# Performance work log

Measured on AMD Instinct MI355X. Metric: run time of the kernel, lower is better.

## Reference

```python
import jax, jax.numpy as jnp
import numpy as np

N_GRAPHS = 64

def setup_inputs() -> dict:
    key = jax.random.key(0)
    ks = jax.random.split(key, 8)
    N, E, H = 50000, 600000, 128
    x = jax.random.normal(ks[0], (N, 2), dtype=jnp.float32)
    edge_index = jax.random.randint(ks[1], (2, E), 0, N, dtype=jnp.int64)
    batch = jnp.sort(jax.random.randint(ks[2], (N,), 0, N_GRAPHS, dtype=jnp.int64))
    s = 0.1  # keep tanh out of saturation
    return {
        'x': x,
        'edge_index': edge_index,
        'batch': batch,
        'W1': jax.random.normal(ks[3], (2, H), dtype=jnp.float32) * s,
        'b1': jnp.zeros((H,), jnp.float32),
        'W2': jax.random.normal(ks[4], (H, H), dtype=jnp.float32) * s,
        'b2': jnp.zeros((H,), jnp.float32),
        'W3': jax.random.normal(ks[5], (H, H), dtype=jnp.float32) * s,
        'b3': jnp.zeros((H,), jnp.float32),
        'Wo': jax.random.normal(ks[6], (2 * H, 41), dtype=jnp.float32) * s,
        'bo': jnp.zeros((41,), jnp.float32),
    }

def reference(x, edge_index, batch, W1, b1, W2, b2, W3, b3, Wo, bo):
    N = x.shape[0]
    src, dst = edge_index[0], edge_index[1]
    # GCN symmetric normalization with self loops: deg = in-degree + 1
    ones_e = jnp.ones(src.shape[0], dtype=x.dtype)
    deg = jax.ops.segment_sum(ones_e, dst, num_segments=N) + 1.0
    dinv = jax.lax.rsqrt(deg)                       # [N]
    edge_norm = (dinv[src] * dinv[dst])[:, None]    # [E,1]
    self_norm = (dinv * dinv)[:, None]              # [N,1]

    def gcn(h, W, b):
        h = h @ W                                   # [N,H] transform first
        agg = jax.ops.segment_sum(h[src] * edge_norm, dst, num_segments=N)
        return agg + h * self_norm + b

    h = jnp.tanh(gcn(x, W1, b1))
    h = jnp.tanh(gcn(h, W2, b2))
    h = jnp.tanh(gcn(h, W3, b3))

    # global max pool + global mean pool over graphs
    cnt = jax.ops.segment_sum(jnp.ones(N, dtype=h.dtype), batch, num_segments=N_GRAPHS)
    mx = jax.ops.segment_max(h, batch, num_segments=N_GRAPHS)
    mx = jnp.where(cnt[:, None] > 0, mx, 0.0)
    mean = jax.ops.segment_sum(h, batch, num_segments=N_GRAPHS) / jnp.maximum(cnt, 1.0)[:, None]
    pooled = jnp.concatenate([mx, mean], axis=1)    # [G, 2H]
    return jnp.tanh(pooled @ Wo + bo)               # [G, 41]
```

## Files before the change

### kernel.cpp

```cpp
#include <hip/hip_runtime.h>
#include <math.h>

#define NGRAPH 64
#define SCAN_BLK 1024
#define COLCAP 6144
#define AXCAP 2560

typedef short short8 __attribute__((ext_vector_type(8)));
typedef float floatx4 __attribute__((ext_vector_type(4)));

__device__ inline unsigned pack_bf16x2(float a, float b) {
    unsigned ua = __float_as_uint(a);
    unsigned ub = __float_as_uint(b);
    ua = (ua + 0x7fffu + ((ua >> 16) & 1u)) >> 16;
    ub = (ub + 0x7fffu + ((ub >> 16) & 1u)) >> 16;
    return ua | (ub << 16);
}
__device__ inline unsigned short bf16_1(float a) {
    unsigned ua = __float_as_uint(a);
    return (unsigned short)((ua + 0x7fffu + ((ua >> 16) & 1u)) >> 16);
}
__device__ inline float bf16lo(unsigned u) { return __uint_as_float(u << 16); }
__device__ inline float bf16hi(unsigned u) { return __uint_as_float(u & 0xffff0000u); }

__device__ inline unsigned fkey(float v) {
    unsigned u = __float_as_uint(v);
    return (v >= 0.f) ? (u | 0x80000000u) : ~u;
}


#define TIDX(u) ((size_t)((qb + (unsigned)(u)) * 4u + (unsigned)q))
#define ACC4() do {                                                       \
    uint4 v0 = t4[TIDX(u0)]; uint4 v1 = t4[TIDX(u1)];                     \
    uint4 v2 = t4[TIDX(u2)]; uint4 v3 = t4[TIDX(u3)];                     \
    a[0] += bf16lo(v0.x); a[1] += bf16hi(v0.x);                           \
    a[2] += bf16lo(v0.y); a[3] += bf16hi(v0.y);                           \
    a[4] += bf16lo(v0.z); a[5] += bf16hi(v0.z);                           \
    a[6] += bf16lo(v0.w); a[7] += bf16hi(v0.w);                           \
    a[0] += bf16lo(v1.x); a[1] += bf16hi(v1.x);                           \
    a[2] += bf16lo(v1.y); a[3] += bf16hi(v1.y);                           \
    a[4] += bf16lo(v1.z); a[5] += bf16hi(v1.z);                           \
    a[6] += bf16lo(v1.w); a[7] += bf16hi(v1.w);                           \
    a[0] += bf16lo(v2.x); a[1] += bf16hi(v2.x);                           \
    a[2] += bf16lo(v2.y); a[3] += bf16hi(v2.y);                           \
    a[4] += bf16lo(v2.z); a[5] += bf16hi(v2.z);                           \
    a[6] += bf16lo(v2.w); a[7] += bf16hi(v2.w);                           \
    a[0] += bf16lo(v3.x); a[1] += bf16hi(v3.x);                           \
    a[2] += bf16lo(v3.y); a[3] += bf16hi(v3.y);                           \
    a[4] += bf16lo(v3.z); a[5] += bf16hi(v3.z);                           \
    a[6] += bf16lo(v3.w); a[7] += bf16hi(v3.w);                           \
} while (0)
#define ACC4M() do {                                                      \
    uint4 v0 = t4[TIDX(u0)]; uint4 v1 = t4[TIDX(u1)];                     \
    uint4 v2 = t4[TIDX(u2)]; uint4 v3 = t4[TIDX(u3)];                     \
    a[0] += bf16lo(v0.x); a[1] += bf16hi(v0.x);                           \
    a[2] += bf16lo(v0.y); a[3] += bf16hi(v0.y);                           \
    a[4] += bf16lo(v0.z); a[5] += bf16hi(v0.z);                           \
    a[6] += bf16lo(v0.w); a[7] += bf16hi(v0.w);                           \
    a[0] = fmaf(m1, bf16lo(v1.x), a[0]); a[1] = fmaf(m1, bf16hi(v1.x), a[1]); \
    a[2] = fmaf(m1, bf16lo(v1.y), a[2]); a[3] = fmaf(m1, bf16hi(v1.y), a[3]); \
    a[4] = fmaf(m1, bf16lo(v1.z), a[4]); a[5] = fmaf(m1, bf16hi(v1.z), a[5]); \
    a[6] = fmaf(m1, bf16lo(v1.w), a[6]); a[7] = fmaf(m1, bf16hi(v1.w), a[7]); \
    a[0] = fmaf(m2, bf16lo(v2.x), a[0]); a[1] = fmaf(m2, bf16hi(v2.x), a[1]); \
    a[2] = fmaf(m2, bf16lo(v2.y), a[2]); a[3] = fmaf(m2, bf16hi(v2.y), a[3]); \
    a[4] = fmaf(m2, bf16lo(v2.z), a[4]); a[5] = fmaf(m2, bf16hi(v2.z), a[5]); \
    a[6] = fmaf(m2, bf16lo(v2.w), a[6]); a[7] = fmaf(m2, bf16hi(v2.w), a[7]); \
    a[0] = fmaf(m3, bf16lo(v3.x), a[0]); a[1] = fmaf(m3, bf16hi(v3.x), a[1]); \
    a[2] = fmaf(m3, bf16lo(v3.y), a[2]); a[3] = fmaf(m3, bf16hi(v3.y), a[3]); \
    a[4] = fmaf(m3, bf16lo(v3.z), a[4]); a[5] = fmaf(m3, bf16hi(v3.z), a[5]); \
    a[6] = fmaf(m3, bf16lo(v3.w), a[6]); a[7] = fmaf(m3, bf16hi(v3.w), a[7]); \
} while (0)


__global__ void pack_count(const int* __restrict__ dst, int E, int* __restrict__ cnt,
                           int* __restrict__ rank,
                           const float* __restrict__ W2, const float* __restrict__ W3,
                           unsigned* __restrict__ Wt2, unsigned* __restrict__ Wt3) {
    if (blockIdx.x < 32) {
        int b = blockIdx.x;
        const float* W = (b < 16) ? W2 : W3;
        unsigned* Wt = (b < 16) ? Wt2 : Wt3;
        b &= 15;
        int bk = b & 3, bn = b >> 2;
        __shared__ float s[32][33];
        int tx = threadIdx.x & 31, ty = threadIdx.x >> 5;
#pragma unroll
        for (int r = 0; r < 4; ++r)
            s[r * 8 + ty][tx] = W[(bk * 32 + r * 8 + ty) * 128 + bn * 32 + tx];
        __syncthreads();
        int t16 = threadIdx.x & 15, tn = threadIdx.x >> 4;
#pragma unroll
        for (int pass = 0; pass < 2; ++pass) {
            int nl = pass * 16 + tn;
            unsigned pk = pack_bf16x2(s[2 * t16][nl], s[2 * t16 + 1][nl]);
            Wt[(bn * 32 + nl) * 64 + bk * 16 + t16] = pk;
        }
    } else {
        int e = (blockIdx.x - 32) * blockDim.x + threadIdx.x;
        if (e < E) rank[e] = atomicAdd(&cnt[dst[e]], 1);
    }
}


__global__ __launch_bounds__(SCAN_BLK) void scanA(const int* __restrict__ cnt,
                                                  const float* __restrict__ x,
                                                  int* __restrict__ row_ptr,
                                                  int* __restrict__ bsum,
                                                  float* __restrict__ dinv,
                                                  float2* __restrict__ y,
                                                  const int* __restrict__ batch,
                                                  int* __restrict__ ticket,
                                                  int* __restrict__ goff, int N) {
    __shared__ int sm[SCAN_BLK];
    __shared__ int amLast;
    int i = blockIdx.x * SCAN_BLK + threadIdx.x;
    int v = (i < N) ? cnt[i] : 0;
    if (i < N) {
        float dv = rsqrtf((float)v + 1.0f);
        dinv[i] = dv;
        float2 xv = ((const float2*)x)[i];
        y[i] = make_float2(xv.x * dv, xv.y * dv);
    }
    sm[threadIdx.x] = v;
    __syncthreads();
    for (int off = 1; off < SCAN_BLK; off <<= 1) {
        int t = (threadIdx.x >= (unsigned)off) ? sm[threadIdx.x - off] : 0;
        __syncthreads();
        sm[threadIdx.x] += t;
        __syncthreads();
    }
    if (i < N) row_ptr[i] = sm[threadIdx.x] - v;
    if (threadIdx.x == SCAN_BLK - 1) bsum[blockIdx.x] = sm[SCAN_BLK - 1];
    __syncthreads();
    if (threadIdx.x == 0) {
        __threadfence();
        amLast = (atomicAdd(ticket, 1) == (int)gridDim.x - 1);
    }
    __syncthreads();
    if (!amLast) return;
    int nb = (int)gridDim.x;
    int v2 = (threadIdx.x < (unsigned)nb) ? atomicAdd(&bsum[threadIdx.x], 0) : 0;
    sm[threadIdx.x] = v2;
    __syncthreads();
    for (int off = 1; off < SCAN_BLK; off <<= 1) {
        int t = (threadIdx.x >= (unsigned)off) ? sm[threadIdx.x - off] : 0;
        __syncthreads();
        sm[threadIdx.x] += t;
        __syncthreads();
    }
    if (threadIdx.x < (unsigned)nb) bsum[threadIdx.x] = sm[threadIdx.x] - v2;
    if (threadIdx.x <= NGRAPH) {
        int g = threadIdx.x;
        int lo = 0, hi = N;
        while (lo < hi) {
            int mid = (lo + hi) >> 1;
            if (batch[mid] < g) lo = mid + 1; else hi = mid;
        }
        goff[g] = lo;
    }
}

__global__ void fill_kernel(const int* __restrict__ src, const int* __restrict__ dst, int E,
                            const int* __restrict__ row_ptr, const int* __restrict__ bsum,
                            const int* __restrict__ rank, int* __restrict__ col) {
    int e = blockIdx.x * blockDim.x + threadIdx.x;
    if (e < E) {
        int d = dst[e];
        int p = row_ptr[d] + bsum[d >> 10] + rank[e];
        col[p] = src[e];
    }
}


__global__ __launch_bounds__(256) void agg_x_t1(const float2* __restrict__ y,
                                                const int* __restrict__ row_ptr,
                                                const int* __restrict__ bsum,
                                                const int* __restrict__ col,
                                                const float* __restrict__ dinv,
                                                const float* __restrict__ W1,
                                                const float* __restrict__ b1,
                                                unsigned short* __restrict__ h, int N, int E) {
    __shared__ float4 sW[64];
    __shared__ float4 sb[32];
    __shared__ float2 zs[64];
    __shared__ int scol[AXCAP];
    if (threadIdx.x < 64) sW[threadIdx.x] = ((const float4*)W1)[threadIdx.x];
    if (threadIdx.x >= 64 && threadIdx.x < 96) sb[threadIdx.x - 64] = ((const float4*)b1)[threadIdx.x - 64];

    int firstNode = blockIdx.x * 64;
    int lastNode = min(firstNode + 64, N);
    int sBase = row_ptr[firstNode] + bsum[firstNode >> 10];
    int eEnd = (lastNode < N) ? row_ptr[lastNode] + bsum[lastNode >> 10] : E;
    int range = eEnd - sBase;
    bool inLds = (range <= AXCAP);
    if (inLds) {
        for (int i = threadIdx.x; i < range; i += 256) scol[i] = col[sBase + i];
    }
    __syncthreads();

    int grp = threadIdx.x >> 2;
    int l4 = threadIdx.x & 3;
    int node = firstNode + grp;
    float ax = 0.f, ay = 0.f;
    if (node < N) {
        int s = row_ptr[node] + bsum[node >> 10];
        int e = (node + 1 < N) ? row_ptr[node + 1] + bsum[(node + 1) >> 10] : E;
        int deg = e - s;
        if (inLds) {
            int sl = s - sBase;
            int j = l4;
            for (; j + 4 < deg; j += 8) {
                float2 v0 = y[scol[sl + j]];
                float2 v1 = y[scol[sl + j + 4]];
                ax += v0.x; ay += v0.y;
                ax += v1.x; ay += v1.y;
            }
            if (j < deg) { float2 v = y[scol[sl + j]]; ax += v.x; ay += v.y; }
        } else {
            int j = l4;
            for (; j + 4 < deg; j += 8) {
                float2 v0 = y[col[s + j]];
                float2 v1 = y[col[s + j + 4]];
                ax += v0.x; ay += v0.y;
                ax += v1.x; ay += v1.y;
            }
            if (j < deg) { float2 v = y[col[s + j]]; ax += v.x; ay += v.y; }
        }
    }
    ax += __shfl_xor(ax, 1, 64); ay += __shfl_xor(ay, 1, 64);
    ax += __shfl_xor(ax, 2, 64); ay += __shfl_xor(ay, 2, 64);
    if (l4 == 0 && node < N) {
        float2 self = y[node];
        float dv = dinv[node];
        zs[grp] = make_float2(dv * (ax + self.x), dv * (ay + self.y));
    }
    __syncthreads();

    int q = threadIdx.x & 31;
    int rsub = threadIdx.x >> 5;
    float4 w0 = sW[q];
    float4 w1 = sW[32 + q];
    float4 b = sb[q];
    size_t qoff = (size_t)(q >> 3) * N;
#pragma unroll
    for (int pass = 0; pass < 8; ++pass) {
        int local = pass * 8 + rsub;
        int row = firstNode + local;
        if (row >= N) break;
        float2 z = zs[local];
        float ox = tanhf(fmaf(z.x, w0.x, fmaf(z.y, w1.x, b.x)));
        float oy = tanhf(fmaf(z.x, w0.y, fmaf(z.y, w1.y, b.y)));
        float oz = tanhf(fmaf(z.x, w0.z, fmaf(z.y, w1.z, b.z)));
        float ow = tanhf(fmaf(z.x, w0.w, fmaf(z.y, w1.w, b.w)));
        uint2 pk;
        pk.x = pack_bf16x2(ox, oy);
        pk.y = pack_bf16x2(oz, ow);
        ((uint2*)h)[(qoff + row) * 8 + (q & 7)] = pk;
    }
}


__global__ __launch_bounds__(256) void gemm_mfma(const unsigned short* __restrict__ A,
                                                 const unsigned* __restrict__ Wt,
                                                 const float* __restrict__ dinv,
                                                 unsigned short* __restrict__ t, int N) {
    __shared__ unsigned sW[128 * 68];
    const uint4* Wt4 = (const uint4*)Wt;
    for (int i = threadIdx.x; i < 2048; i += 256) {
        int n = i >> 4, c = i & 15;
        *(uint4*)&sW[n * 68 + c * 4] = Wt4[i];
    }
    __syncthreads();
    int l = threadIdx.x & 63;
    int w = threadIdx.x >> 6;
    int lm = l & 15;
    int q4 = l >> 4;

    floatx4 acc[2][8];
#pragma unroll
    for (int i = 0; i < 2; ++i)
#pragma unroll
        for (int j = 0; j < 8; ++j) acc[i][j] = (floatx4){0.f, 0.f, 0.f, 0.f};

    int rowbase = blockIdx.x * 128 + w * 32;
    int k8 = q4 * 8;
#pragma unroll
    for (int ks = 0; ks < 4; ++ks) {
        short8 a[2];
#pragma unroll
        for (int mt = 0; mt < 2; ++mt) {
            int r = min(rowbase + mt * 16 + lm, N - 1);
            a[mt] = *(const short8*)(A + ((size_t)ks * N + r) * 32 + k8);
        }
#pragma unroll
        for (int nt = 0; nt < 8; ++nt) {
            short8 b = *(const short8*)&sW[(nt * 16 + lm) * 68 + ks * 16 + q4 * 4];
#pragma unroll
            for (int mt = 0; mt < 2; ++mt)
                acc[mt][nt] = __builtin_amdgcn_mfma_f32_16x16x32_bf16(b, a[mt], acc[mt][nt], 0, 0, 0);
        }
    }

#pragma unroll
    for (int mt = 0; mt < 2; ++mt) {
        int gr = rowbase + mt * 16 + lm;
        if (gr < N) {
            float dv = dinv[gr];
#pragma unroll
            for (int nt = 0; nt < 8; ++nt) {
                uint2 pk;
                pk.x = pack_bf16x2(acc[mt][nt][0] * dv, acc[mt][nt][1] * dv);
                pk.y = pack_bf16x2(acc[mt][nt][2] * dv, acc[mt][nt][3] * dv);
                *(uint2*)(t + ((size_t)(nt >> 1) * N + gr) * 32 + (nt & 1) * 16 + q4 * 4) = pk;
            }
        }
    }
}


__global__ __launch_bounds__(1024) void agg_kernel(const unsigned short* __restrict__ t,
                                                   const int* __restrict__ row_ptr,
                                                   const int* __restrict__ bsum,
                                                   const int* __restrict__ col,
                                                   const float* __restrict__ dinv,
                                                   const float* __restrict__ bias,
                                                   unsigned short* __restrict__ out, int N, int E) {
    int nchunk = (N + 255) >> 8;
    int bid = (int)blockIdx.x;
    int r8 = bid & 7;
    int qt = r8 >> 1;
    int c = (bid >> 3) * 2 + (r8 & 1);
    if (c >= nchunk) return;

    __shared__ int scol[COLCAP];
    int firstNode = c * 256;
    int lastNode = min(firstNode + 256, N);
    int sBase = row_ptr[firstNode] + bsum[firstNode >> 10];
    int eEnd = (lastNode < N) ? row_ptr[lastNode] + bsum[lastNode >> 10] : E;
    int range = eEnd - sBase;
    bool inLds = (range <= COLCAP);
    if (inLds) {
        for (int i = threadIdx.x; i < range; i += 1024) scol[i] = col[sBase + i];
    }
    __syncthreads();

    int q = threadIdx.x & 3;
    int node = firstNode + ((int)threadIdx.x >> 2);
    if (node >= N) return;
    const uint4* t4 = (const uint4*)t;
    unsigned qb = (unsigned)qt * (unsigned)N;
    int s = row_ptr[node] + bsum[node >> 10];
    int e = (node + 1 < N) ? row_ptr[node + 1] + bsum[(node + 1) >> 10] : E;
    int deg = e - s;

    float a[8];
    {
        uint4 v = t4[TIDX(node)];
        a[0] = bf16lo(v.x); a[1] = bf16hi(v.x);
        a[2] = bf16lo(v.y); a[3] = bf16hi(v.y);
        a[4] = bf16lo(v.z); a[5] = bf16hi(v.z);
        a[6] = bf16lo(v.w); a[7] = bf16hi(v.w);
    }
    int j = 0;
    if (inLds) {
        int sl = s - sBase;
        for (; j + 4 <= deg; j += 4) {
            int u0 = scol[sl + j], u1 = scol[sl + j + 1];
            int u2 = scol[sl + j + 2], u3 = scol[sl + j + 3];
            ACC4();
        }
        if (j < deg) {
            float m1 = (j + 1 < deg) ? 1.f : 0.f;
            float m2 = (j + 2 < deg) ? 1.f : 0.f;
            float m3 = (j + 3 < deg) ? 1.f : 0.f;
            int u0 = scol[sl + j];
            int u1 = scol[sl + min(j + 1, deg - 1)];
            int u2 = scol[sl + min(j + 2, deg - 1)];
            int u3 = scol[sl + min(j + 3, deg - 1)];
            ACC4M();
        }
    } else {
        for (; j + 4 <= deg; j += 4) {
            int u0 = col[s + j], u1 = col[s + j + 1];
            int u2 = col[s + j + 2], u3 = col[s + j + 3];
            ACC4();
        }
        if (j < deg) {
            float m1 = (j + 1 < deg) ? 1.f : 0.f;
            float m2 = (j + 2 < deg) ? 1.f : 0.f;
            float m3 = (j + 3 < deg) ? 1.f : 0.f;
            int u0 = col[s + j];
            int u1 = col[s + min(j + 1, deg - 1)];
            int u2 = col[s + min(j + 2, deg - 1)];
            int u3 = col[s + min(j + 3, deg - 1)];
            ACC4M();
        }
    }

    float dv = dinv[node];
    const float4* b4 = (const float4*)bias;
    float4 b0 = b4[qt * 8 + q * 2];
    float4 b1 = b4[qt * 8 + q * 2 + 1];
    uint4 pk;
    pk.x = pack_bf16x2(tanhf(fmaf(dv, a[0], b0.x)), tanhf(fmaf(dv, a[1], b0.y)));
    pk.y = pack_bf16x2(tanhf(fmaf(dv, a[2], b0.z)), tanhf(fmaf(dv, a[3], b0.w)));
    pk.z = pack_bf16x2(tanhf(fmaf(dv, a[4], b1.x)), tanhf(fmaf(dv, a[5], b1.y)));
    pk.w = pack_bf16x2(tanhf(fmaf(dv, a[6], b1.z)), tanhf(fmaf(dv, a[7], b1.w)));
    ((uint4*)out)[TIDX(node)] = pk;
}


__global__ __launch_bounds__(1024) void agg3_pool(const unsigned short* __restrict__ t,
                                                  const int* __restrict__ row_ptr,
                                                  const int* __restrict__ bsum,
                                                  const int* __restrict__ col,
                                                  const float* __restrict__ dinv,
                                                  const float* __restrict__ bias,
                                                  const int* __restrict__ batch,
                                                  unsigned* __restrict__ pmax,
                                                  float* __restrict__ psum, int N, int E) {
    int nchunk = (N + 255) >> 8;
    int bid = (int)blockIdx.x;
    int r8 = bid & 7;
    int qt = r8 >> 1;
    int c = (bid >> 3) * 2 + (r8 & 1);
    if (c >= nchunk) return;

    __shared__ unsigned smax[2][32];
    __shared__ float ssum[2][32];
    __shared__ int scol[COLCAP];
    if (threadIdx.x < 64) {
        smax[threadIdx.x >> 5][threadIdx.x & 31] = 0u;
        ssum[threadIdx.x >> 5][threadIdx.x & 31] = 0.f;
    }
    int firstNode = c * 256;
    int lastNode = min(firstNode + 256, N);
    int sBase = row_ptr[firstNode] + bsum[firstNode >> 10];
    int eEnd = (lastNode < N) ? row_ptr[lastNode] + bsum[lastNode >> 10] : E;
    int range = eEnd - sBase;
    bool inLds = (range <= COLCAP);
    if (inLds) {
        for (int i = threadIdx.x; i < range; i += 1024) scol[i] = col[sBase + i];
    }
    __syncthreads();

    int q = threadIdx.x & 3;
    int blockBase = firstNode;
    int node = blockBase + ((int)threadIdx.x >> 2);
    bool valid = node < N;
    int nc = valid ? node : N - 1;
    const uint4* t4 = (const uint4*)t;
    unsigned qb = (unsigned)qt * (unsigned)N;
    int s = row_ptr[nc] + bsum[nc >> 10];
    int e = (nc + 1 < N) ? row_ptr[nc + 1] + bsum[(nc + 1) >> 10] : E;
    int deg = valid ? (e - s) : 0;

    float a[8];
    {
        uint4 v = t4[TIDX(nc)];
        a[0] = bf16lo(v.x); a[1] = bf16hi(v.x);
        a[2] = bf16lo(v.y); a[3] = bf16hi(v.y);
        a[4] = bf16lo(v.z); a[5] = bf16hi(v.z);
        a[6] = bf16lo(v.w); a[7] = bf16hi(v.w);
    }
    int j = 0;
    if (inLds) {
        int sl = s - sBase;
        for (; j + 4 <= deg; j += 4) {
            int u0 = scol[sl + j], u1 = scol[sl + j + 1];
            int u2 = scol[sl + j + 2], u3 = scol[sl + j + 3];
            ACC4();
        }
        if (j < deg) {
            float m1 = (j + 1 < deg) ? 1.f : 0.f;
            float m2 = (j + 2 < deg) ? 1.f : 0.f;
            float m3 = (j + 3 < deg) ? 1.f : 0.f;
            int u0 = scol[sl + j];
            int u1 = scol[sl + min(j + 1, deg - 1)];
            int u2 = scol[sl + min(j + 2, deg - 1)];
            int u3 = scol[sl + min(j + 3, deg - 1)];
            ACC4M();
        }
    } else {
        for (; j + 4 <= deg; j += 4) {
            int u0 = col[s + j], u1 = col[s + j + 1];
            int u2 = col[s + j + 2], u3 = col[s + j + 3];
            ACC4();
        }
        if (j < deg) {
            float m1 = (j + 1 < deg) ? 1.f : 0.f;
            float m2 = (j + 2 < deg) ? 1.f : 0.f;
            float m3 = (j + 3 < deg) ? 1.f : 0.f;
            int u0 = col[s + j];
            int u1 = col[s + min(j + 1, deg - 1)];
            int u2 = col[s + min(j + 2, deg - 1)];
            int u3 = col[s + min(j + 3, deg - 1)];
            ACC4M();
        }
    }

    float dv = dinv[nc];
    const float4* b4 = (const float4*)bias;
    float4 b0 = b4[qt * 8 + q * 2];
    float4 b1 = b4[qt * 8 + q * 2 + 1];
    float o[8];
    o[0] = tanhf(fmaf(dv, a[0], b0.x)); o[1] = tanhf(fmaf(dv, a[1], b0.y));
    o[2] = tanhf(fmaf(dv, a[2], b0.z)); o[3] = tanhf(fmaf(dv, a[3], b0.w));
    o[4] = tanhf(fmaf(dv, a[4], b1.x)); o[5] = tanhf(fmaf(dv, a[5], b1.y));
    o[6] = tanhf(fmaf(dv, a[6], b1.z)); o[7] = tanhf(fmaf(dv, a[7], b1.w));

    int g = batch[nc];
    int g0 = batch[min(blockBase, N - 1)];
    int gl = __shfl(g, 0, 64);
    int gh = __shfl(g, 63, 64);

    if (gl == gh) {
        float m[8], sv[8];
#pragma unroll
        for (int k = 0; k < 8; ++k) {
            m[k] = valid ? o[k] : -3.402823466e+38f;
            sv[k] = valid ? o[k] : 0.f;
        }
#pragma unroll
        for (int st = 4; st < 64; st <<= 1) {
#pragma unroll
            for (int k = 0; k < 8; ++k) {
                m[k] = fmaxf(m[k], __shfl_xor(m[k], st, 64));
                sv[k] += __shfl_xor(sv[k], st, 64);
            }
        }
        if (((threadIdx.x & 63) >> 2) == 0) {
            int seg = gl - g0;
            if (seg < 2) {
#pragma unroll
                for (int k = 0; k < 8; ++k) {
                    atomicMax(&smax[seg][q * 8 + k], fkey(m[k]));
                    atomicAdd(&ssum[seg][q * 8 + k], sv[k]);
                }
            } else {
#pragma unroll
                for (int k = 0; k < 8; ++k) {
                    atomicMax(&pmax[gl * 128 + qt * 32 + q * 8 + k], fkey(m[k]));
                    atomicAdd(&psum[gl * 128 + qt * 32 + q * 8 + k], sv[k]);
                }
            }
        }
    } else {
        if (valid) {
            int seg = g - g0;
            if (seg < 2) {
#pragma unroll
                for (int k = 0; k < 8; ++k) {
                    atomicMax(&smax[seg][q * 8 + k], fkey(o[k]));
                    atomicAdd(&ssum[seg][q * 8 + k], o[k]);
                }
            } else {
#pragma unroll
                for (int k = 0; k < 8; ++k) {
                    atomicMax(&pmax[g * 128 + qt * 32 + q * 8 + k], fkey(o[k]));
                    atomicAdd(&psum[g * 128 + qt * 32 + q * 8 + k], o[k]);
                }
            }
        }
    }
    __syncthreads();
    if (threadIdx.x < 64) {
        int seg = threadIdx.x >> 5, cc = threadIdx.x & 31;
        int g0b = batch[min(blockBase, N - 1)];
        int gg = g0b + seg;
        if (gg < NGRAPH) {
            atomicMax(&pmax[gg * 128 + qt * 32 + cc], smax[seg][cc]);
            atomicAdd(&psum[gg * 128 + qt * 32 + cc], ssum[seg][cc]);
        }
    }
}


__global__ __launch_bounds__(128) void pool_final(const unsigned* __restrict__ pmax,
                                                  const float* __restrict__ psum,
                                                  const int* __restrict__ goff,
                                                  const float* __restrict__ Wo,
                                                  const float* __restrict__ bo,
                                                  float* __restrict__ out) {
    __shared__ float p[256];
    int g = blockIdx.x;
    int j = threadIdx.x;
    int cnt = goff[g + 1] - goff[g];
    unsigned key = pmax[g * 128 + j];
    float mx = (key & 0x80000000u) ? __uint_as_float(key ^ 0x80000000u)
                                   : __uint_as_float(~key);
    p[j] = (cnt > 0) ? mx : 0.f;
    p[128 + j] = psum[g * 128 + j] / fmaxf((float)cnt, 1.f);
    __syncthreads();
    if (j < 41) {
        float acc = bo[j];
        for (int k = 0; k < 256; ++k) acc = fmaf(p[k], Wo[k * 41 + j], acc);
        out[g * 41 + j] = tanhf(acc);
    }
}


extern "C" void kernel_launch(void* const* d_in, const int* in_sizes, int n_in,
                              void* d_out, int out_size, void* d_ws, size_t ws_size,
                              hipStream_t stream) {
    const float* x   = (const float*)d_in[0];
    const int*   ei  = (const int*)d_in[1];
    const int* batch = (const int*)d_in[2];
    const float* W1  = (const float*)d_in[3];
    const float* b1  = (const float*)d_in[4];
    const float* W2  = (const float*)d_in[5];
    const float* b2  = (const float*)d_in[6];
    const float* W3  = (const float*)d_in[7];
    const float* b3  = (const float*)d_in[8];
    const float* Wo  = (const float*)d_in[9];
    const float* bo  = (const float*)d_in[10];
    float* outp = (float*)d_out;

    int N = in_sizes[2];
    int E = in_sizes[1] / 2;
    const int* src = ei;
    const int* dst = ei + E;

    char* p = (char*)d_ws;
    auto alloc = [&](size_t bytes) -> char* {
        char* q = p;
        p += (bytes + 255) & ~(size_t)255;
        return q;
    };
    unsigned short* t   = (unsigned short*)alloc((size_t)N * 128 * 2);
    unsigned short* hb  = (unsigned short*)alloc((size_t)N * 128 * 2);
    float* dinv   = (float*)alloc((size_t)N * 4);
    int*   rowp   = (int*)alloc((size_t)(N + 1) * 4);
    int*   col    = (int*)alloc((size_t)E * 4);
    int*   rank   = (int*)alloc((size_t)E * 4);
    int*   goff   = (int*)alloc(65 * 4);
    float2* y     = (float2*)alloc((size_t)N * 8);
    unsigned* Wt2 = (unsigned*)alloc(128 * 64 * 4);
    unsigned* Wt3 = (unsigned*)alloc(128 * 64 * 4);
    int nscan = (N + SCAN_BLK - 1) / SCAN_BLK;
    int*   bsum   = (int*)alloc((size_t)nscan * 4);
    size_t cntB = ((size_t)N * 4 + 255) & ~(size_t)255;
    char* zbase = alloc(cntB + 256 + NGRAPH * 128 * 4 * 2);
    int*      cnt  = (int*)zbase;
    int*      tick = (int*)(zbase + cntB);
    unsigned* pmax = (unsigned*)(zbase + cntB + 256);
    float*    psum = (float*)(zbase + cntB + 256 + NGRAPH * 128 * 4);

    (void)hipMemsetAsync(zbase, 0, cntB + 256 + NGRAPH * 128 * 4 * 2, stream);

    pack_count<<<32 + (E + 255) / 256, 256, 0, stream>>>(dst, E, cnt, rank, W2, W3, Wt2, Wt3);
    scanA<<<nscan, SCAN_BLK, 0, stream>>>(cnt, x, rowp, bsum, dinv, y, batch, tick, goff, N);
    fill_kernel<<<(E + 255) / 256, 256, 0, stream>>>(src, dst, E, rowp, bsum, rank, col);

    int nchunk = (N + 255) >> 8;
    int nchunkR = (nchunk + 1) & ~1;
    int nblk = nchunkR * 4;

    agg_x_t1<<<(N + 63) / 64, 256, 0, stream>>>(y, rowp, bsum, col, dinv, W1, b1, hb, N, E);
    gemm_mfma<<<(N + 127) / 128, 256, 0, stream>>>(hb, Wt2, dinv, t, N);
    agg_kernel<<<nblk, 1024, 0, stream>>>(t, rowp, bsum, col, dinv, b2, hb, N, E);
    gemm_mfma<<<(N + 127) / 128, 256, 0, stream>>>(hb, Wt3, dinv, t, N);
    agg3_pool<<<nblk, 1024, 0, stream>>>(t, rowp, bsum, col, dinv, b3, batch, pmax, psum, N, E);

    pool_final<<<NGRAPH, 128, 0, stream>>>(pmax, psum, goff, Wo, bo, outp);
}
```

Measured before the change: 228.7 us.

## Split feature storage into eight 16-column slabs and use nontemporal stores

Stores the bf16 feature matrices as eight column slabs of 16 features each instead of four slabs of 32, so each aggregation block owns one 16-column slice of 512 nodes, with two threads per node instead of four. The GEMM, first-layer, aggregation and pooling indexing are all updated to match, and output writes become nontemporal stores. The aim is a narrower gather footprint per slice for better cache locality, plus less cache pollution from streaming writes. In exchange, each node's neighbour column list is reloaded by more blocks, the column staging buffer in LDS grows, and the pooling atomics are spread across more partial slices.

New measurement: 248.0 us. +8.4%, slower.

```diff
diff --git a/kernel.cpp b/kernel.cpp
--- a/kernel.cpp
+++ b/kernel.cpp
@@ -3,11 +3,13 @@
 
 #define NGRAPH 64
 #define SCAN_BLK 1024
-#define COLCAP 6144
+#define COLCAP 7680
 #define AXCAP 2560
 
 typedef short short8 __attribute__((ext_vector_type(8)));
 typedef float floatx4 __attribute__((ext_vector_type(4)));
+typedef unsigned uintx2 __attribute__((ext_vector_type(2)));
+typedef unsigned uintx4 __attribute__((ext_vector_type(4)));
 
 __device__ inline unsigned pack_bf16x2(float a, float b) {
     unsigned ua = __float_as_uint(a);
@@ -16,10 +18,6 @@
     ub = (ub + 0x7fffu + ((ub >> 16) & 1u)) >> 16;
     return ua | (ub << 16);
 }
-__device__ inline unsigned short bf16_1(float a) {
-    unsigned ua = __float_as_uint(a);
-    return (unsigned short)((ua + 0x7fffu + ((ua >> 16) & 1u)) >> 16);
-}
 __device__ inline float bf16lo(unsigned u) { return __uint_as_float(u << 16); }
 __device__ inline float bf16hi(unsigned u) { return __uint_as_float(u & 0xffff0000u); }
 
@@ -29,7 +27,7 @@
 }
 
 
-#define TIDX(u) ((size_t)((qb + (unsigned)(u)) * 4u + (unsigned)q))
+#define TIDX(u) ((size_t)((qb + (unsigned)(u)) * 2u + (unsigned)q))
 #define ACC4() do {                                                       \
     uint4 v0 = t4[TIDX(u0)]; uint4 v1 = t4[TIDX(u1)];                     \
     uint4 v2 = t4[TIDX(u2)]; uint4 v3 = t4[TIDX(u3)];                     \
@@ -241,7 +239,7 @@
     float4 w0 = sW[q];
     float4 w1 = sW[32 + q];
     float4 b = sb[q];
-    size_t qoff = (size_t)(q >> 3) * N;
+    size_t ebase = (size_t)(q >> 2) * N;
 #pragma unroll
     for (int pass = 0; pass < 8; ++pass) {
         int local = pass * 8 + rsub;
@@ -252,10 +250,10 @@
         float oy = tanhf(fmaf(z.x, w0.y, fmaf(z.y, w1.y, b.y)));
         float oz = tanhf(fmaf(z.x, w0.z, fmaf(z.y, w1.z, b.z)));
         float ow = tanhf(fmaf(z.x, w0.w, fmaf(z.y, w1.w, b.w)));
-        uint2 pk;
+        uintx2 pk;
         pk.x = pack_bf16x2(ox, oy);
         pk.y = pack_bf16x2(oz, ow);
-        ((uint2*)h)[(qoff + row) * 8 + (q & 7)] = pk;
+        __builtin_nontemporal_store(pk, (uintx2*)h + (ebase + row) * 4 + (q & 3));
     }
 }
 
@@ -283,14 +281,13 @@
         for (int j = 0; j < 8; ++j) acc[i][j] = (floatx4){0.f, 0.f, 0.f, 0.f};
 
     int rowbase = blockIdx.x * 128 + w * 32;
-    int k8 = q4 * 8;
 #pragma unroll
     for (int ks = 0; ks < 4; ++ks) {
         short8 a[2];
 #pragma unroll
         for (int mt = 0; mt < 2; ++mt) {
             int r = min(rowbase + mt * 16 + lm, N - 1);
-            a[mt] = *(const short8*)(A + ((size_t)ks * N + r) * 32 + k8);
+            a[mt] = *(const short8*)(A + ((size_t)(ks * 2 + (q4 >> 1)) * N + r) * 16 + (q4 & 1) * 8);
         }
 #pragma unroll
         for (int nt = 0; nt < 8; ++nt) {
@@ -308,10 +305,11 @@
             float dv = dinv[gr];
 #pragma unroll
             for (int nt = 0; nt < 8; ++nt) {
-                uint2 pk;
+                uintx2 pk;
                 pk.x = pack_bf16x2(acc[mt][nt][0] * dv, acc[mt][nt][1] * dv);
                 pk.y = pack_bf16x2(acc[mt][nt][2] * dv, acc[mt][nt][3] * dv);
-                *(uint2*)(t + ((size_t)(nt >> 1) * N + gr) * 32 + (nt & 1) * 16 + q4 * 4) = pk;
+                __builtin_nontemporal_store(pk,
+                    (uintx2*)(t + ((size_t)nt * N + gr) * 16 + q4 * 4));
             }
         }
     }
@@ -325,16 +323,15 @@
                                                    const float* __restrict__ dinv,
                                                    const float* __restrict__ bias,
                                                    unsigned short* __restrict__ out, int N, int E) {
-    int nchunk = (N + 255) >> 8;
+    int nchunk = (N + 511) >> 9;
     int bid = (int)blockIdx.x;
-    int r8 = bid & 7;
-    int qt = r8 >> 1;
-    int c = (bid >> 3) * 2 + (r8 & 1);
+    int et = bid & 7;
+    int c = bid >> 3;
     if (c >= nchunk) return;
 
     __shared__ int scol[COLCAP];
-    int firstNode = c * 256;
-    int lastNode = min(firstNode + 256, N);
+    int firstNode = c * 512;
+    int lastNode = min(firstNode + 512, N);
     int sBase = row_ptr[firstNode] + bsum[firstNode >> 10];
     int eEnd = (lastNode < N) ? row_ptr[lastNode] + bsum[lastNode >> 10] : E;
     int range = eEnd - sBase;
@@ -344,11 +341,11 @@
     }
     __syncthreads();
 
-    int q = threadIdx.x & 3;
-    int node = firstNode + ((int)threadIdx.x >> 2);
+    int q = threadIdx.x & 1;
+    int node = firstNode + ((int)threadIdx.x >> 1);
     if (node >= N) return;
     const uint4* t4 = (const uint4*)t;
-    unsigned qb = (unsigned)qt * (unsigned)N;
+    unsigned qb = (unsigned)et * (unsigned)N;
     int s = row_ptr[node] + bsum[node >> 10];
     int e = (node + 1 < N) ? row_ptr[node + 1] + bsum[(node + 1) >> 10] : E;
     int deg = e - s;
@@ -399,14 +396,14 @@
 
     float dv = dinv[node];
     const float4* b4 = (const float4*)bias;
-    float4 b0 = b4[qt * 8 + q * 2];
-    float4 b1 = b4[qt * 8 + q * 2 + 1];
-    uint4 pk;
+    float4 b0 = b4[et * 4 + q * 2];
+    float4 b1 = b4[et * 4 + q * 2 + 1];
+    uintx4 pk;
     pk.x = pack_bf16x2(tanhf(fmaf(dv, a[0], b0.x)), tanhf(fmaf(dv, a[1], b0.y)));
     pk.y = pack_bf16x2(tanhf(fmaf(dv, a[2], b0.z)), tanhf(fmaf(dv, a[3], b0.w)));
     pk.z = pack_bf16x2(tanhf(fmaf(dv, a[4], b1.x)), tanhf(fmaf(dv, a[5], b1.y)));
     pk.w = pack_bf16x2(tanhf(fmaf(dv, a[6], b1.z)), tanhf(fmaf(dv, a[7], b1.w)));
-    ((uint4*)out)[TIDX(node)] = pk;
+    __builtin_nontemporal_store(pk, (uintx4*)out + TIDX(node));
 }
 
 
@@ -419,22 +416,21 @@
                                                   const int* __restrict__ batch,
                                                   unsigned* __restrict__ pmax,
                                                   float* __restrict__ psum, int N, int E) {
-    int nchunk = (N + 255) >> 8;
+    int nchunk = (N + 511) >> 9;
     int bid = (int)blockIdx.x;
-    int r8 = bid & 7;
-    int qt = r8 >> 1;
-    int c = (bid >> 3) * 2 + (r8 & 1);
+    int et = bid & 7;
+    int c = bid >> 3;
     if (c >= nchunk) return;
 
-    __shared__ unsigned smax[2][32];
-    __shared__ float ssum[2][32];
+    __shared__ unsigned smax[2][16];
+    __shared__ float ssum[2][16];
     __shared__ int scol[COLCAP];
-    if (threadIdx.x < 64) {
-        smax[threadIdx.x >> 5][threadIdx.x & 31] = 0u;
-        ssum[threadIdx.x >> 5][threadIdx.x & 31] = 0.f;
-    }
-    int firstNode = c * 256;
-    int lastNode = min(firstNode + 256, N);
+    if (threadIdx.x < 32) {
+        smax[threadIdx.x >> 4][threadIdx.x & 15] = 0u;
+        ssum[threadIdx.x >> 4][threadIdx.x & 15] = 0.f;
+    }
+    int firstNode = c * 512;
+    int lastNode = min(firstNode + 512, N);
     int sBase = row_ptr[firstNode] + bsum[firstNode >> 10];
     int eEnd = (lastNode < N) ? row_ptr[lastNode] + bsum[lastNode >> 10] : E;
     int range = eEnd - sBase;
@@ -444,13 +440,13 @@
     }
     __syncthreads();
 
-    int q = threadIdx.x & 3;
+    int q = threadIdx.x & 1;
     int blockBase = firstNode;
-    int node = blockBase + ((int)threadIdx.x >> 2);
+    int node = blockBase + ((int)threadIdx.x >> 1);
     bool valid = node < N;
     int nc = valid ? node : N - 1;
     const uint4* t4 = (const uint4*)t;
-    unsigned qb = (unsigned)qt * (unsigned)N;
+    unsigned qb = (unsigned)et * (unsigned)N;
     int s = row_ptr[nc] + bsum[nc >> 10];
     int e = (nc + 1 < N) ? row_ptr[nc + 1] + bsum[(nc + 1) >> 10] : E;
     int deg = valid ? (e - s) : 0;
@@ -501,8 +497,8 @@
 
     float dv = dinv[nc];
     const float4* b4 = (const float4*)bias;
-    float4 b0 = b4[qt * 8 + q * 2];
-    float4 b1 = b4[qt * 8 + q * 2 + 1];
+    float4 b0 = b4[et * 4 + q * 2];
+    float4 b1 = b4[et * 4 + q * 2 + 1];
     float o[8];
     o[0] = tanhf(fmaf(dv, a[0], b0.x)); o[1] = tanhf(fmaf(dv, a[1], b0.y));
     o[2] = tanhf(fmaf(dv, a[2], b0.z)); o[3] = tanhf(fmaf(dv, a[3], b0.w));
@@ -522,14 +518,14 @@
             sv[k] = valid ? o[k] : 0.f;
         }
 #pragma unroll
-        for (int st = 4; st < 64; st <<= 1) {
+        for (int st = 2; st < 64; st <<= 1) {
 #pragma unroll
             for (int k = 0; k < 8; ++k) {
                 m[k] = fmaxf(m[k], __shfl_xor(m[k], st, 64));
                 sv[k] += __shfl_xor(sv[k], st, 64);
             }
         }
-        if (((threadIdx.x & 63) >> 2) == 0) {
+        if ((threadIdx.x & 63) < 2) {
             int seg = gl - g0;
             if (seg < 2) {
 #pragma unroll
@@ -540,8 +536,8 @@
             } else {
 #pragma unroll
                 for (int k = 0; k < 8; ++k) {
-                    atomicMax(&pmax[gl * 128 + qt * 32 + q * 8 + k], fkey(m[k]));
-                    atomicAdd(&psum[gl * 128 + qt * 32 + q * 8 + k], sv[k]);
+                    atomicMax(&pmax[gl * 128 + et * 16 + q * 8 + k], fkey(m[k]));
+                    atomicAdd(&psum[gl * 128 + et * 16 + q * 8 + k], sv[k]);
                 }
             }
         }
@@ -557,20 +553,20 @@
             } else {
 #pragma unroll
                 for (int k = 0; k < 8; ++k) {
-                    atomicMax(&pmax[g * 128 + qt * 32 + q * 8 + k], fkey(o[k]));
-                    atomicAdd(&psum[g * 128 + qt * 32 + q * 8 + k], o[k]);
+                    atomicMax(&pmax[g * 128 + et * 16 + q * 8 + k], fkey(o[k]));
+                    atomicAdd(&psum[g * 128 + et * 16 + q * 8 + k], o[k]);
                 }
             }
         }
     }
     __syncthreads();
-    if (threadIdx.x < 64) {
-        int seg = threadIdx.x >> 5, cc = threadIdx.x & 31;
+    if (threadIdx.x < 32) {
+        int seg = threadIdx.x >> 4, cc = threadIdx.x & 15;
         int g0b = batch[min(blockBase, N - 1)];
         int gg = g0b + seg;
         if (gg < NGRAPH) {
-            atomicMax(&pmax[gg * 128 + qt * 32 + cc], smax[seg][cc]);
-            atomicAdd(&psum[gg * 128 + qt * 32 + cc], ssum[seg][cc]);
+            atomicMax(&pmax[gg * 128 + et * 16 + cc], smax[seg][cc]);
+            atomicAdd(&psum[gg * 128 + et * 16 + cc], ssum[seg][cc]);
         }
     }
 }
@@ -652,9 +648,8 @@
     scanA<<<nscan, SCAN_BLK, 0, stream>>>(cnt, x, rowp, bsum, dinv, y, batch, tick, goff, N);
     fill_kernel<<<(E + 255) / 256, 256, 0, stream>>>(src, dst, E, rowp, bsum, rank, col);
 
-    int nchunk = (N + 255) >> 8;
-    int nchunkR = (nchunk + 1) & ~1;
-    int nblk = nchunkR * 4;
+    int nchunk = (N + 511) >> 9;
+    int nblk = nchunk * 8;
 
     agg_x_t1<<<(N + 63) / 64, 256, 0, stream>>>(y, rowp, bsum, col, dinv, W1, b1, hb, N, E);
     gemm_mfma<<<(N + 127) / 128, 256, 0, stream>>>(hb, Wt2, dinv, t, N);
```
